# Kernel tuning notes

Hardware: AMD Instinct MI355X
Metric: run time of the kernel (lower is better)

The kernel has to match this reference:

```python
import jax, jax.numpy as jnp
import numpy as np

HEADS = 8
DIM_HEAD = 64
MAX_REL = 200  # max_rel_dist


def setup_inputs() -> dict:
    key = jax.random.key(0)
    ks = jax.random.split(key, 5)
    B, N, D = 4, 2048, 512
    x = jax.random.normal(ks[0], (B, N, D), dtype=jnp.float32)
    temporal_mask = jax.random.randint(ks[1], (N, N), 0, 2, dtype=jnp.int32)
    gamma = jnp.ones((D,), jnp.float32)
    beta = jnp.zeros((D,), jnp.float32)
    Wqkv = jax.random.normal(ks[2], (D, 3 * HEADS * DIM_HEAD), dtype=jnp.float32) * 0.02
    Wout = jax.random.normal(ks[3], (HEADS * DIM_HEAD, D), dtype=jnp.float32) * 0.02
    bout = jnp.zeros((D,), jnp.float32)
    rel_table = jax.random.normal(ks[4], (2 * MAX_REL - 1,), dtype=jnp.float32) * 0.02
    return {"x": x, "gamma": gamma, "beta": beta, "Wqkv": Wqkv, "Wout": Wout,
            "bout": bout, "rel_table": rel_table, "temporal_mask": temporal_mask}


def reference(x, gamma, beta, Wqkv, Wout, bout, rel_table, temporal_mask):
    B, N, D = x.shape
    scale = DIM_HEAD ** -0.5
    # LayerNorm
    mu = jnp.mean(x, axis=-1, keepdims=True)
    var = jnp.mean(jnp.square(x - mu), axis=-1, keepdims=True)
    xn = (x - mu) * jax.lax.rsqrt(var + 1e-5) * gamma + beta
    # QKV projection (no bias), split heads: b n (h d) -> b h n d
    qkv = xn @ Wqkv  # [B, N, 3*H*d]
    q, k, v = jnp.split(qkv, 3, axis=-1)
    split = lambda t: t.reshape(B, N, HEADS, DIM_HEAD).transpose(0, 2, 1, 3)
    q, k, v = split(q), split(k), split(v)
    # scores with learned relative-position bias
    dots = jnp.einsum('bhnd,bhmd->bhnm', q, k) * scale  # [B,H,N,N]
    idx = jnp.arange(N)
    rel = jnp.clip(idx[:, None] - idx[None, :], -(MAX_REL - 1), MAX_REL - 1) + MAX_REL - 1
    dots = dots + rel_table[rel][None, None, :, :]
    # temporal mask (0 -> -inf); large negative for grad safety
    dots = jnp.where(temporal_mask[None, None, :, :] == 0, jnp.float32(-1e9), dots)
    attn = jax.nn.softmax(dots, axis=-1)
    out = jnp.einsum('bhnm,bhmd->bhnd', attn, v)
    out = out.transpose(0, 2, 1, 3).reshape(B, N, HEADS * DIM_HEAD)
    return out @ Wout + bout
```

## Files before the change

kernel.cpp:

```cpp
#include <hip/hip_runtime.h>

typedef __attribute__((ext_vector_type(8))) short bf16x8;
typedef __attribute__((ext_vector_type(4))) short bf16x4;
typedef __attribute__((ext_vector_type(4))) float f32x4;
typedef unsigned short ushort_t;

#define B_ 4
#define H_ 8
#define N_ 2048
#define D_ 512
#define MAXREL 199
#define LOG2E 1.4426950408889634f

__device__ __forceinline__ ushort_t f2bf(float f) {
    union { float f; unsigned u; } v; v.f = f;
    unsigned r = v.u + 0x7fffu + ((v.u >> 16) & 1u);
    return (ushort_t)(r >> 16);
}
__device__ __forceinline__ float bf2f(ushort_t u) {
    union { unsigned u; float f; } v; v.u = ((unsigned)u) << 16;
    return v.f;
}
__device__ __forceinline__ float fexp2(float x) {
#if __has_builtin(__builtin_amdgcn_exp2f)
    return __builtin_amdgcn_exp2f(x);
#else
    return __expf(x * 0.6931471805599453f);
#endif
}
__device__ __forceinline__ unsigned cvt_pk_bf16(float lo, float hi) {
    unsigned r;
    asm("v_cvt_pk_bf16_f32 %0, %1, %2" : "=v"(r) : "v"(lo), "v"(hi));
    return r;
}
__device__ __forceinline__ void gl_lds16(const ushort_t* g, ushort_t* l) {
    __builtin_amdgcn_global_load_lds(
        (const __attribute__((address_space(1))) void*)g,
        (__attribute__((address_space(3))) void*)l,
        16, 0, 0);
}

#define PREP_LN    2048
#define PREP_WQ    768
#define PREP_WO    256
__global__ __launch_bounds__(256) void prep_kernel(const float* __restrict__ x,
                                                   const float* __restrict__ gamma,
                                                   const float* __restrict__ beta,
                                                   ushort_t* __restrict__ xn,
                                                   const float* __restrict__ Wqkv,
                                                   ushort_t* __restrict__ WqkvT,
                                                   const float* __restrict__ Wout,
                                                   ushort_t* __restrict__ WoutT) {
    __shared__ float smem[32 * 33];
    const int blk = blockIdx.x;
    const int t = threadIdx.x;

    if (blk < PREP_LN) {
        const int row = blk * 4 + (t >> 6);
        const int l = t & 63;
        const float* xr = x + (size_t)row * D_;
        float4 a = *(const float4*)&xr[l * 4];
        float4 c = *(const float4*)&xr[256 + l * 4];
        float s = (a.x + a.y) + (a.z + a.w) + (c.x + c.y) + (c.z + c.w);
        #pragma unroll
        for (int o = 1; o < 64; o <<= 1) s += __shfl_xor(s, o);
        float mu = s * (1.0f / D_);
        float dx0 = a.x - mu, dx1 = a.y - mu, dx2 = a.z - mu, dx3 = a.w - mu;
        float dy0 = c.x - mu, dy1 = c.y - mu, dy2 = c.z - mu, dy3 = c.w - mu;
        float s2 = dx0*dx0 + dx1*dx1 + dx2*dx2 + dx3*dx3
                 + dy0*dy0 + dy1*dy1 + dy2*dy2 + dy3*dy3;
        #pragma unroll
        for (int o = 1; o < 64; o <<= 1) s2 += __shfl_xor(s2, o);
        float rs = rsqrtf(s2 * (1.0f / D_) + 1e-5f);
        float4 g1 = *(const float4*)&gamma[l * 4];
        float4 g2 = *(const float4*)&gamma[256 + l * 4];
        float4 b1 = *(const float4*)&beta[l * 4];
        float4 b2 = *(const float4*)&beta[256 + l * 4];
        ushort_t* yr = xn + (size_t)row * D_;
        union { ushort_t us[4]; unsigned long long ll; } o1, o2;
        o1.us[0] = f2bf(dx0 * rs * g1.x + b1.x);
        o1.us[1] = f2bf(dx1 * rs * g1.y + b1.y);
        o1.us[2] = f2bf(dx2 * rs * g1.z + b1.z);
        o1.us[3] = f2bf(dx3 * rs * g1.w + b1.w);
        o2.us[0] = f2bf(dy0 * rs * g2.x + b2.x);
        o2.us[1] = f2bf(dy1 * rs * g2.y + b2.y);
        o2.us[2] = f2bf(dy2 * rs * g2.z + b2.z);
        o2.us[3] = f2bf(dy3 * rs * g2.w + b2.w);
        *(unsigned long long*)(yr + l * 4) = o1.ll;
        *(unsigned long long*)(yr + 256 + l * 4) = o2.ll;
    } else {
        const float* W; ushort_t* Wt; int Nn, i;
        if (blk < PREP_LN + PREP_WQ) {
            i = blk - PREP_LN; W = Wqkv; Wt = WqkvT; Nn = 1536;
        } else {
            i = blk - (PREP_LN + PREP_WQ); W = Wout; Wt = WoutT; Nn = 512;
        }
        const int nb = Nn >> 5;
        const int bx = (i % nb) * 32, by = (i / nb) * 32;
        const int tx = t & 31, ty = t >> 5;
        float (*tile)[33] = (float(*)[33])smem;
        #pragma unroll
        for (int k = 0; k < 32; k += 8)
            tile[ty + k][tx] = W[(size_t)(by + ty + k) * Nn + bx + tx];
        __syncthreads();
        #pragma unroll
        for (int k = 0; k < 32; k += 8)
            Wt[(size_t)(bx + ty + k) * 512 + by + tx] = f2bf(tile[tx][ty + k]);
    }
}

#define QKV_BIAS_BLKS 128
__global__ __launch_bounds__(256) void gemm_qkv(const ushort_t* __restrict__ A,
                                                const ushort_t* __restrict__ Bt,
                                                ushort_t* __restrict__ qb,
                                                ushort_t* __restrict__ kb,
                                                ushort_t* __restrict__ vb,
                                                const float* __restrict__ rel,
                                                const int* __restrict__ mask,
                                                ushort_t* __restrict__ bp) {
    __shared__ ushort_t As[2][4096];
    __shared__ ushort_t Bs[2][4096];
    const int bid = blockIdx.x;
    const int t = threadIdx.x;

    if (bid < QKV_BIAS_BLKS) {
        unsigned long long (*lds_t)[16][17] = (unsigned long long(*)[16][17])As;
        const int w = t >> 6, l = t & 63;
        const int n0 = bid * 16;
        const int m4 = l & 15;
        const int m4d = ((l >> 4) << 2) | ((l >> 2) & 3);
        const size_t rbase0 = (((size_t)(bid >> 3)) << 18) + (((size_t)(bid & 7)) << 10);
        #pragma unroll
        for (int i = 0; i < 8; i++) {
            const int jt = w + i * 4;
            const int m = jt * 64 + m4 * 4;
            #pragma unroll
            for (int s = 0; s < 4; s++) {
                const int nl = s * 4 + (l >> 4);
                const int n = n0 + nl;
                const int4 mv = *(const int4*)&mask[(size_t)n * 2048 + m];
                union { ushort_t us[4]; unsigned long long ll; } pkv;
                #pragma unroll
                for (int j = 0; j < 4; j++) {
                    int dl = n - (m + j);
                    dl = dl < -MAXREL ? -MAXREL : (dl > MAXREL ? MAXREL : dl);
                    int mj = (j == 0) ? mv.x : (j == 1) ? mv.y : (j == 2) ? mv.z : mv.w;
                    float v = (mj == 0) ? -1e9f : rel[dl + MAXREL] * LOG2E;
                    pkv.us[j] = f2bf(v);
                }
                lds_t[w][nl][m4] = pkv.ll;
            }
            ushort_t* dst = bp + rbase0 + ((size_t)jt << 13) + (size_t)l * 16;
            union { unsigned long long q[2]; bf16x8 v; } s0, s1;
            s0.q[0] = lds_t[w][4 * (l & 3) + 0][m4d];
            s0.q[1] = lds_t[w][4 * (l & 3) + 1][m4d];
            s1.q[0] = lds_t[w][4 * (l & 3) + 2][m4d];
            s1.q[1] = lds_t[w][4 * (l & 3) + 3][m4d];
            *(bf16x8*)(dst) = s0.v;
            *(bf16x8*)(dst + 8) = s1.v;
        }
        return;
    }

    const int gid = bid - QKV_BIAS_BLKS;
    const int lane = t & 63, w = t >> 6;
    const int m16 = lane & 15, quad = lane >> 4;
    const int wr = w >> 1, wc = w & 1;
    const int r0 = (gid / 12) * 128, c0 = (gid % 12) * 128;

    const ushort_t* Ag = A  + (size_t)(r0 + (t >> 2)) * D_ + (t & 3) * 8;
    const ushort_t* Bg = Bt + (size_t)(c0 + (t >> 2)) * D_ + (t & 3) * 8;

    f32x4 acc[4][4];
    #pragma unroll
    for (int i = 0; i < 4; i++)
        #pragma unroll
        for (int j = 0; j < 4; j++) acc[i][j] = (f32x4){0.f, 0.f, 0.f, 0.f};

    gl_lds16(Ag, As[0] + w * 512);
    gl_lds16(Ag + (size_t)64 * D_, As[0] + w * 512 + 2048);
    gl_lds16(Bg, Bs[0] + w * 512);
    gl_lds16(Bg + (size_t)64 * D_, Bs[0] + w * 512 + 2048);
    __syncthreads();

    for (int k0 = 0; k0 < D_; k0 += 32) {
        const int buf = (k0 >> 5) & 1;
        if (k0 + 32 < D_) {
            gl_lds16(Ag + k0 + 32, As[buf ^ 1] + w * 512);
            gl_lds16(Ag + k0 + 32 + (size_t)64 * D_, As[buf ^ 1] + w * 512 + 2048);
            gl_lds16(Bg + k0 + 32, Bs[buf ^ 1] + w * 512);
            gl_lds16(Bg + k0 + 32 + (size_t)64 * D_, Bs[buf ^ 1] + w * 512 + 2048);
        }
        bf16x8 af[4], bfr[4];
        #pragma unroll
        for (int rt = 0; rt < 4; rt++)
            af[rt] = *(const bf16x8*)(As[buf] + (wr * 64 + rt * 16 + m16) * 32 + quad * 8);
        #pragma unroll
        for (int ct = 0; ct < 4; ct++)
            bfr[ct] = *(const bf16x8*)(Bs[buf] + (wc * 64 + ct * 16 + m16) * 32 + quad * 8);
        #pragma unroll
        for (int rt = 0; rt < 4; rt++)
            #pragma unroll
            for (int ct = 0; ct < 4; ct++)
                acc[rt][ct] = __builtin_amdgcn_mfma_f32_16x16x32_bf16(af[rt], bfr[ct], acc[rt][ct], 0, 0, 0);
        __syncthreads();
    }

    const int b_blk = r0 >> 11, n_base = r0 & 2047;
    if ((c0 >> 9) == 2) {
        ushort_t* SH = As[0];
        #pragma unroll
        for (int ph = 0; ph < 2; ph++) {
            if (ph) __syncthreads();
            if (wc == ph) {
                #pragma unroll
                for (int ct = 0; ct < 4; ct++) {
                    int dcol = ct * 16 + m16;
                    #pragma unroll
                    for (int rt = 0; rt < 4; rt++) {
                        int nl = wr * 64 + rt * 16 + quad * 4;
                        union { ushort_t us[4]; unsigned long long ll; } pkv;
                        #pragma unroll
                        for (int r = 0; r < 4; r++) pkv.us[r] = f2bf(acc[rt][ct][r]);
                        *(unsigned long long*)(&SH[dcol * 128 + (nl ^ ((dcol & 7) << 3))]) = pkv.ll;
                    }
                }
            }
            __syncthreads();
            int h = ((c0 + ph * 64) >> 6) & 7;
            #pragma unroll
            for (int p = 0; p < 4; p++) {
                int dr = p * 16 + (t >> 4);
                int n0 = (t & 15) * 8;
                bf16x8 vv = *(const bf16x8*)&SH[dr * 128 + (n0 ^ ((dr & 7) << 3))];
                *(bf16x8*)(vb + ((size_t)(b_blk * H_ + h) * 64 + dr) * N_ + n_base + n0) = vv;
            }
        }
    } else {
        #pragma unroll
        for (int ct = 0; ct < 4; ct++) {
            int cc = c0 + wc * 64 + ct * 16;
            int which = cc >> 9;
            int h = (cc >> 6) & 7;
            int d = (cc & 63) + m16;
            #pragma unroll
            for (int rt = 0; rt < 4; rt++) {
                int rowb = r0 + wr * 64 + rt * 16 + quad * 4;
                int b = rowb >> 11, n0 = rowb & 2047;
                if (which == 0) {
                    #pragma unroll
                    for (int r = 0; r < 4; r++)
                        qb[((size_t)((b * H_ + h) * N_ + n0 + r)) * 64 + d] = f2bf(acc[rt][ct][r] * (0.125f * LOG2E));
                } else {
                    #pragma unroll
                    for (int r = 0; r < 4; r++)
                        kb[((size_t)((b * H_ + h) * N_ + n0 + r)) * 64 + d] = f2bf(acc[rt][ct][r]);
                }
            }
        }
    }
}

__global__ __launch_bounds__(256) void gemm_out(const ushort_t* __restrict__ A,
                                                const ushort_t* __restrict__ Bt,
                                                const float* __restrict__ bias,
                                                float* __restrict__ C) {
    __shared__ ushort_t As[2][2048];
    __shared__ ushort_t Bs[2][4096];
    const int t = threadIdx.x;
    const int lane = t & 63, w = t >> 6;
    const int m16 = lane & 15, quad = lane >> 4;
    const int wr = w >> 1, wc = w & 1;
    const int r0 = blockIdx.y * 64, c0 = blockIdx.x * 128;

    const ushort_t* Ag = A  + (size_t)(r0 + (t >> 2)) * D_ + (t & 3) * 8;
    const ushort_t* Bg = Bt + (size_t)(c0 + (t >> 2)) * D_ + (t & 3) * 8;

    f32x4 acc[2][4];
    #pragma unroll
    for (int i = 0; i < 2; i++)
        #pragma unroll
        for (int j = 0; j < 4; j++) acc[i][j] = (f32x4){0.f, 0.f, 0.f, 0.f};

    gl_lds16(Ag, As[0] + w * 512);
    gl_lds16(Bg, Bs[0] + w * 512);
    gl_lds16(Bg + (size_t)64 * D_, Bs[0] + w * 512 + 2048);
    __syncthreads();

    for (int k0 = 0; k0 < D_; k0 += 32) {
        const int buf = (k0 >> 5) & 1;
        if (k0 + 32 < D_) {
            gl_lds16(Ag + k0 + 32, As[buf ^ 1] + w * 512);
            gl_lds16(Bg + k0 + 32, Bs[buf ^ 1] + w * 512);
            gl_lds16(Bg + k0 + 32 + (size_t)64 * D_, Bs[buf ^ 1] + w * 512 + 2048);
        }
        bf16x8 af[2], bfr[4];
        #pragma unroll
        for (int mf = 0; mf < 2; mf++)
            af[mf] = *(const bf16x8*)(As[buf] + (wr * 32 + mf * 16 + m16) * 32 + quad * 8);
        #pragma unroll
        for (int nt = 0; nt < 4; nt++)
            bfr[nt] = *(const bf16x8*)(Bs[buf] + (wc * 64 + nt * 16 + m16) * 32 + quad * 8);
        #pragma unroll
        for (int mf = 0; mf < 2; mf++)
            #pragma unroll
            for (int nt = 0; nt < 4; nt++)
                acc[mf][nt] = __builtin_amdgcn_mfma_f32_16x16x32_bf16(af[mf], bfr[nt], acc[mf][nt], 0, 0, 0);
        __syncthreads();
    }

    #pragma unroll
    for (int mf = 0; mf < 2; mf++) {
        #pragma unroll
        for (int nt = 0; nt < 4; nt++) {
            int col = c0 + wc * 64 + nt * 16 + m16;
            int row0 = r0 + wr * 32 + mf * 16 + quad * 4;
            float bv = bias[col];
            #pragma unroll
            for (int r = 0; r < 4; r++)
                C[(size_t)(row0 + r) * 512 + col] = acc[mf][nt][r] + bv;
        }
    }
}

#define ATTN_TILE(JT, KCUR, VCUR, KNXT, VNXT, BCUR, BNXT)                              \
  {                                                                                    \
    const int jt = (JT);                                                               \
    const int buf = jt & 1;                                                            \
    if (jt + 2 < 32) {                                                                 \
      KNXT = *(const bf16x8*)(kgbase + (size_t)((jt + 2) * 64 + srow) * 64 + scb * 8); \
      VNXT = *(const bf16x8*)(vgbase + (size_t)srow * N_ + (jt + 2) * 64 + scb * 8);   \
    }                                                                                  \
    if (jt + 1 < 32) {                                                                 \
      _Pragma("unroll")                                                                \
      for (int nt = 0; nt < 4; nt++)                                                   \
        BNXT[nt] = *(const bf16x4*)(bpb + ((jt + 1) << 13) + (nt << 8));               \
    }                                                                                  \
    unsigned pk[8];                                                                    \
    __builtin_amdgcn_s_setprio(1);                                                     \
    _Pragma("unroll")                                                                  \
    for (int nt = 0; nt < 4; nt++) {                                                   \
      f32x4 a2;                                                                        \
      _Pragma("unroll")                                                                \
      for (int r = 0; r < 4; r++) a2[r] = bf2f((ushort_t)BCUR[nt][r]);                 \
      int kr = nt * 16 + m16;                                                          \
      bf16x8 kf0 = *(const bf16x8*)(&Ks[buf][kr * 64 + ((quad) ^ (kr & 7)) * 8]);      \
      bf16x8 kf1 = *(const bf16x8*)(&Ks[buf][kr * 64 + ((quad + 4) ^ (kr & 7)) * 8]);  \
      a2 = __builtin_amdgcn_mfma_f32_16x16x32_bf16(kf0, qa0, a2, 0, 0, 0);             \
      a2 = __builtin_amdgcn_mfma_f32_16x16x32_bf16(kf1, qa1, a2, 0, 0, 0);             \
      float p0 = fexp2(a2[0]), p1 = fexp2(a2[1]);                                      \
      float p2 = fexp2(a2[2]), p3 = fexp2(a2[3]);                                      \
      pk[nt * 2]     = cvt_pk_bf16(p0, p1);                                            \
      pk[nt * 2 + 1] = cvt_pk_bf16(p2, p3);                                            \
    }                                                                                  \
    __builtin_amdgcn_s_setprio(0);                                                     \
    _Pragma("unroll")                                                                  \
    for (int i = 0; i < 4; i++) {                                                      \
      int chunk = 2 * i + (quad >> 1);                                                 \
      union { unsigned uu[2]; unsigned long long ll; } wrp;                            \
      wrp.uu[0] = pk[2 * i]; wrp.uu[1] = pk[2 * i + 1];                                \
      *(unsigned long long*)(pw + m16 * 64 + ((chunk ^ (m16 & 7)) << 3)                \
                             + (quad & 1) * 4) = wrp.ll;                               \
    }                                                                                  \
    bf16x8 pa0 = *(const bf16x8*)(pw + m16 * 64 + ((quad ^ (m16 & 7)) << 3));          \
    bf16x8 pa1 = *(const bf16x8*)(pw + m16 * 64 + (((quad + 4) ^ (m16 & 7)) << 3));    \
    __builtin_amdgcn_s_setprio(1);                                                     \
    rs = __builtin_amdgcn_mfma_f32_16x16x32_bf16(pa0, kones, rs, 0, 0, 0);             \
    rs = __builtin_amdgcn_mfma_f32_16x16x32_bf16(pa1, kones, rs, 0, 0, 0);             \
    _Pragma("unroll")                                                                  \
    for (int nt = 0; nt < 4; nt++) {                                                   \
      int d = nt * 16 + m16;                                                           \
      bf16x8 vf0 = *(const bf16x8*)(&Vs[buf][d * 64 + ((quad) ^ (d & 7)) * 8]);        \
      bf16x8 vf1 = *(const bf16x8*)(&Vs[buf][d * 64 + ((quad + 4) ^ (d & 7)) * 8]);    \
      o[nt] = __builtin_amdgcn_mfma_f32_16x16x32_bf16(pa0, vf0, o[nt], 0, 0, 0);       \
      o[nt] = __builtin_amdgcn_mfma_f32_16x16x32_bf16(pa1, vf1, o[nt], 0, 0, 0);       \
    }                                                                                  \
    __builtin_amdgcn_s_setprio(0);                                                     \
    if (jt + 1 < 32) {                                                                 \
      *(bf16x8*)(&Ks[buf ^ 1][soff]) = KCUR;                                           \
      *(bf16x8*)(&Vs[buf ^ 1][soff]) = VCUR;                                           \
    }                                                                                  \
    __syncthreads();                                                                   \
  }

__global__ __launch_bounds__(512, 4) void attn_mfma(const ushort_t* __restrict__ qb,
                                                    const ushort_t* __restrict__ kb,
                                                    const ushort_t* __restrict__ vb,
                                                    const ushort_t* __restrict__ bp,
                                                    ushort_t* __restrict__ attn) {
    __shared__ ushort_t Ks[2][64 * 64];
    __shared__ ushort_t Vs[2][64 * 64];
    __shared__ ushort_t p_s[8][16 * 64];

    const int t = threadIdx.x;
    const int w = t >> 6, lane = t & 63;
    const int m16 = lane & 15, quad = lane >> 4;
    const int id = blockIdx.x;
    const int bh = id & 31;
    const int qt = id >> 5;
    const int b = bh >> 3, h = bh & 7;
    const int n0w = qt * 128 + w * 16;

    const int srow = t >> 3, scb = t & 7;
    const int soff = srow * 64 + (scb ^ (srow & 7)) * 8;
    const ushort_t* kgbase = kb + ((size_t)bh * N_) * 64;
    const ushort_t* vgbase = vb + ((size_t)bh * 64) * N_;

    const ushort_t* qpb = qb + ((size_t)(bh * N_ + n0w + m16)) * 64 + quad * 8;
    bf16x8 qa0 = *(const bf16x8*)(qpb);
    bf16x8 qa1 = *(const bf16x8*)(qpb + 32);

    const ushort_t* bpb = bp + ((size_t)qt << 18) + (w << 10) + (quad << 6) + (m16 << 2);

    bf16x8 kones;
    #pragma unroll
    for (int i = 0; i < 8; i++) kones[i] = (short)0x3F80;

    *(bf16x8*)(&Ks[0][soff]) = *(const bf16x8*)(kgbase + (size_t)srow * 64 + scb * 8);
    *(bf16x8*)(&Vs[0][soff]) = *(const bf16x8*)(vgbase + (size_t)srow * N_ + scb * 8);
    bf16x8 kA = *(const bf16x8*)(kgbase + (size_t)(64 + srow) * 64 + scb * 8);
    bf16x8 vA = *(const bf16x8*)(vgbase + (size_t)srow * N_ + 64 + scb * 8);
    bf16x8 kB, vB;
    bf16x4 bA[4], bB[4];
    #pragma unroll
    for (int nt = 0; nt < 4; nt++) bA[nt] = *(const bf16x4*)(bpb + (nt << 8));
    __syncthreads();

    f32x4 o[4];
    #pragma unroll
    for (int nt = 0; nt < 4; nt++) o[nt] = (f32x4){0.f, 0.f, 0.f, 0.f};
    f32x4 rs = (f32x4){0.f, 0.f, 0.f, 0.f};

    ushort_t* pw = p_s[w];

    for (int jt2 = 0; jt2 < 16; jt2++) {
        ATTN_TILE(2 * jt2,     kA, vA, kB, vB, bA, bB);
        ATTN_TILE(2 * jt2 + 1, kB, vB, kA, vA, bB, bA);
    }

    #pragma unroll
    for (int r = 0; r < 4; r++) {
        float inv = 1.0f / rs[r];
        int n = n0w + quad * 4 + r;
        ushort_t* orow = attn + ((size_t)(b * N_ + n)) * 512 + h * 64 + m16;
        #pragma unroll
        for (int nt = 0; nt < 4; nt++) orow[nt * 16] = f2bf(o[nt][r] * inv);
    }
}

extern "C" void kernel_launch(void* const* d_in, const int* in_sizes, int n_in,
                              void* d_out, int out_size, void* d_ws, size_t ws_size,
                              hipStream_t stream) {
    const float* x     = (const float*)d_in[0];
    const float* gamma = (const float*)d_in[1];
    const float* beta  = (const float*)d_in[2];
    const float* Wqkv  = (const float*)d_in[3];
    const float* Wout  = (const float*)d_in[4];
    const float* bout  = (const float*)d_in[5];
    const float* rel   = (const float*)d_in[6];
    const int*   mask  = (const int*)d_in[7];
    float* out = (float*)d_out;

    char* wsb = (char*)d_ws;
    ushort_t* xn    = (ushort_t*)(wsb);
    ushort_t* attnb = (ushort_t*)(wsb + ( 8u << 20));
    ushort_t* qb    = (ushort_t*)(wsb + (16u << 20));
    ushort_t* kb    = (ushort_t*)(wsb + (24u << 20));
    ushort_t* vb    = (ushort_t*)(wsb + (32u << 20));
    ushort_t* WqkvT = (ushort_t*)(wsb + (40u << 20));
    ushort_t* WoutT = (ushort_t*)(wsb + (42u << 20));
    ushort_t* bp    = (ushort_t*)(wsb + (44u << 20));

    prep_kernel<<<PREP_LN + PREP_WQ + PREP_WO, 256, 0, stream>>>(
        x, gamma, beta, xn, Wqkv, WqkvT, Wout, WoutT);

    gemm_qkv<<<QKV_BIAS_BLKS + 768, 256, 0, stream>>>(xn, WqkvT, qb, kb, vb, rel, mask, bp);

    attn_mfma<<<512, 512, 0, stream>>>(qb, kb, vb, bp, attnb);

    gemm_out<<<dim3(512 / 128, 8192 / 64), 256, 0, stream>>>(attnb, WoutT, bout, out);
}
```

Measured before the change: 195.3 us.

## Simplify bias-table build and swizzle GEMM block order for XCD locality

Result: no change. 193.0 us (-1.2%).

```diff
diff --git a/kernel.cpp b/kernel.cpp
--- a/kernel.cpp
+++ b/kernel.cpp
@@ -109,7 +109,7 @@
     }
 }
 
-#define QKV_BIAS_BLKS 128
+#define QKV_BIAS_BLKS 512
 __global__ __launch_bounds__(256) void gemm_qkv(const ushort_t* __restrict__ A,
                                                 const ushort_t* __restrict__ Bt,
                                                 ushort_t* __restrict__ qb,
@@ -118,55 +118,40 @@
                                                 const float* __restrict__ rel,
                                                 const int* __restrict__ mask,
                                                 ushort_t* __restrict__ bp) {
+    const int bid = blockIdx.x;
+    const int t = threadIdx.x;
+
+    if (bid < QKV_BIAS_BLKS) {
+        const int base = bid * 8192;
+        #pragma unroll
+        for (int p = 0; p < 8; p++) {
+            int idx = base + p * 1024 + t * 4;
+            int n = idx >> 11, m = idx & 2047;
+            const int4 mv = *(const int4*)&mask[idx];
+            union { ushort_t us[4]; unsigned long long ll; } pkv;
+            #pragma unroll
+            for (int j = 0; j < 4; j++) {
+                int dl = n - (m + j);
+                dl = dl < -MAXREL ? -MAXREL : (dl > MAXREL ? MAXREL : dl);
+                int mj = (j == 0) ? mv.x : (j == 1) ? mv.y : (j == 2) ? mv.z : mv.w;
+                float v = (mj == 0) ? -1e9f : rel[dl + MAXREL] * LOG2E;
+                pkv.us[j] = f2bf(v);
+            }
+            int off = ((n >> 7) << 18) + ((m >> 6) << 13) + (((n >> 4) & 7) << 10)
+                    + (((m >> 4) & 3) << 8) + (((m >> 2) & 3) << 6) + ((n & 15) << 2);
+            *(unsigned long long*)(bp + off) = pkv.ll;
+        }
+        return;
+    }
+
     __shared__ ushort_t As[2][4096];
     __shared__ ushort_t Bs[2][4096];
-    const int bid = blockIdx.x;
-    const int t = threadIdx.x;
-
-    if (bid < QKV_BIAS_BLKS) {
-        unsigned long long (*lds_t)[16][17] = (unsigned long long(*)[16][17])As;
-        const int w = t >> 6, l = t & 63;
-        const int n0 = bid * 16;
-        const int m4 = l & 15;
-        const int m4d = ((l >> 4) << 2) | ((l >> 2) & 3);
-        const size_t rbase0 = (((size_t)(bid >> 3)) << 18) + (((size_t)(bid & 7)) << 10);
-        #pragma unroll
-        for (int i = 0; i < 8; i++) {
-            const int jt = w + i * 4;
-            const int m = jt * 64 + m4 * 4;
-            #pragma unroll
-            for (int s = 0; s < 4; s++) {
-                const int nl = s * 4 + (l >> 4);
-                const int n = n0 + nl;
-                const int4 mv = *(const int4*)&mask[(size_t)n * 2048 + m];
-                union { ushort_t us[4]; unsigned long long ll; } pkv;
-                #pragma unroll
-                for (int j = 0; j < 4; j++) {
-                    int dl = n - (m + j);
-                    dl = dl < -MAXREL ? -MAXREL : (dl > MAXREL ? MAXREL : dl);
-                    int mj = (j == 0) ? mv.x : (j == 1) ? mv.y : (j == 2) ? mv.z : mv.w;
-                    float v = (mj == 0) ? -1e9f : rel[dl + MAXREL] * LOG2E;
-                    pkv.us[j] = f2bf(v);
-                }
-                lds_t[w][nl][m4] = pkv.ll;
-            }
-            ushort_t* dst = bp + rbase0 + ((size_t)jt << 13) + (size_t)l * 16;
-            union { unsigned long long q[2]; bf16x8 v; } s0, s1;
-            s0.q[0] = lds_t[w][4 * (l & 3) + 0][m4d];
-            s0.q[1] = lds_t[w][4 * (l & 3) + 1][m4d];
-            s1.q[0] = lds_t[w][4 * (l & 3) + 2][m4d];
-            s1.q[1] = lds_t[w][4 * (l & 3) + 3][m4d];
-            *(bf16x8*)(dst) = s0.v;
-            *(bf16x8*)(dst + 8) = s1.v;
-        }
-        return;
-    }
-
-    const int gid = bid - QKV_BIAS_BLKS;
+    const int g = bid - QKV_BIAS_BLKS;
+    const int tid = (g & 7) * 96 + (g >> 3);
     const int lane = t & 63, w = t >> 6;
     const int m16 = lane & 15, quad = lane >> 4;
     const int wr = w >> 1, wc = w & 1;
-    const int r0 = (gid / 12) * 128, c0 = (gid % 12) * 128;
+    const int r0 = (tid / 12) * 128, c0 = (tid % 12) * 128;
 
     const ushort_t* Ag = A  + (size_t)(r0 + (t >> 2)) * D_ + (t & 3) * 8;
     const ushort_t* Bg = Bt + (size_t)(c0 + (t >> 2)) * D_ + (t & 3) * 8;
@@ -271,7 +256,8 @@
     const int lane = t & 63, w = t >> 6;
     const int m16 = lane & 15, quad = lane >> 4;
     const int wr = w >> 1, wc = w & 1;
-    const int r0 = blockIdx.y * 64, c0 = blockIdx.x * 128;
+    const int bswz = (blockIdx.x & 7) * 64 + (blockIdx.x >> 3);
+    const int r0 = (bswz >> 2) * 64, c0 = (bswz & 3) * 128;
 
     const ushort_t* Ag = A  + (size_t)(r0 + (t >> 2)) * D_ + (t & 3) * 8;
     const ushort_t* Bg = Bt + (size_t)(c0 + (t >> 2)) * D_ + (t & 3) * 8;
@@ -478,5 +464,5 @@
 
     attn_mfma<<<512, 512, 0, stream>>>(qb, kb, vb, bp, attnb);
 
-    gemm_out<<<dim3(512 / 128, 8192 / 64), 256, 0, stream>>>(attnb, WoutT, bout, out);
-}
+    gemm_out<<<512, 256, 0, stream>>>(attnb, WoutT, bout, out);
+}
```
